# Kernel optimization log

Measured on AMD Instinct MI355X. Metric: run time of the kernel, lower is better.

Reference implementation:

```python
import jax, jax.numpy as jnp
import numpy as np

HEADS = 16
DIM_HEAD = 64
MAX_REL_POS = 1024   # temporal_length
TEXT_LEN = 77
IMG_SCALE = 1.0      # image_cross_attention_scale


def setup_inputs() -> dict:
    key = jax.random.key(0)
    ks = jax.random.split(key, 12)
    B, N, D = 32, 1024, 1024
    CTX = TEXT_LEN + 256
    s = 0.02
    return {
        "x": jax.random.normal(ks[0], (B, N, D), jnp.float32),
        "context": jax.random.normal(ks[1], (B, CTX, D), jnp.float32),
        "W_q": jax.random.normal(ks[2], (D, D), jnp.float32) * s,
        "W_k": jax.random.normal(ks[3], (D, D), jnp.float32) * s,
        "W_v": jax.random.normal(ks[4], (D, D), jnp.float32) * s,
        "W_k_ip": jax.random.normal(ks[5], (D, D), jnp.float32) * s,
        "W_v_ip": jax.random.normal(ks[6], (D, D), jnp.float32) * s,
        "rel_k": jax.random.normal(ks[7], (2 * MAX_REL_POS + 1, DIM_HEAD), jnp.float32) * s,
        "rel_v": jax.random.normal(ks[8], (2 * MAX_REL_POS + 1, DIM_HEAD), jnp.float32) * s,
        "W_out": jax.random.normal(ks[9], (D, D), jnp.float32) * s,
        "b_out": jnp.zeros((D,), jnp.float32),
        "alpha": jnp.zeros((1,), jnp.float32),
    }


def _split_heads(t):
    # [b, n, h*d] -> [b, h, n, d]
    b, n, _ = t.shape
    return t.reshape(b, n, HEADS, DIM_HEAD).transpose(0, 2, 1, 3)


def _merge_heads(t):
    # [b, h, n, d] -> [b, n, h*d]
    b, h, n, d = t.shape
    return t.transpose(0, 2, 1, 3).reshape(b, n, h * d)


def _rel_embeddings(table, len_q, len_k):
    # gather relative-position embeddings: [len_q, len_k, d]
    dist = jnp.arange(len_k)[None, :] - jnp.arange(len_q)[:, None]
    idx = jnp.clip(dist, -MAX_REL_POS, MAX_REL_POS) + MAX_REL_POS
    return table[idx]


def reference(x, context, W_q, W_k, W_v, W_k_ip, W_v_ip, rel_k, rel_v, W_out, b_out, alpha):
    scale = DIM_HEAD ** -0.5
    ctx_text = context[:, :TEXT_LEN, :]
    ctx_img = context[:, TEXT_LEN:, :]

    q = _split_heads(x @ W_q)          # [b,h,i,d]
    k = _split_heads(ctx_text @ W_k)   # [b,h,j,d]
    v = _split_heads(ctx_text @ W_v)

    sim = jnp.einsum('bhid,bhjd->bhij', q, k) * scale
    len_q, len_k = q.shape[2], k.shape[2]
    k2 = _rel_embeddings(rel_k, len_q, len_k)            # [i,j,d]
    sim = sim + jnp.einsum('bhid,ijd->bhij', q, k2) * scale
    attn = jax.nn.softmax(sim, axis=-1)

    out = jnp.einsum('bhij,bhjd->bhid', attn, v)
    v2 = _rel_embeddings(rel_v, len_q, len_k)            # [i,j,d]
    out = out + jnp.einsum('bhij,ijd->bhid', attn, v2)
    out = _merge_heads(out)                              # [b,i,h*d]

    # second image-context KV stream
    k_ip = _split_heads(ctx_img @ W_k_ip)
    v_ip = _split_heads(ctx_img @ W_v_ip)
    sim_ip = jnp.einsum('bhid,bhjd->bhij', q, k_ip) * scale
    attn_ip = jax.nn.softmax(sim_ip, axis=-1)
    out_ip = _merge_heads(jnp.einsum('bhij,bhjd->bhid', attn_ip, v_ip))

    # learnable-scale bypass: out + scale * out_ip * (tanh(alpha)+1)
    out = out + IMG_SCALE * out_ip * (jnp.tanh(alpha[0]) + 1.0)
    return out @ W_out + b_out
```

## Files before the change

### kernel.cpp

```cpp
#include <hip/hip_runtime.h>
#include <math.h>

typedef __bf16 bf16_t;
typedef __bf16 bf16x2 __attribute__((ext_vector_type(2)));
typedef __bf16 bf16x8 __attribute__((ext_vector_type(8)));
typedef float f32x4 __attribute__((ext_vector_type(4)));

#define BATCH   32
#define SEQ     1024
#define DMODEL  1024
#define NHEADS  16
#define DIMH    64
#define TEXTLEN 77
#define IMGLEN  256
#define CTXLEN  333
#define MAXREL  1024

#define MFMA16(a,b,c) __builtin_amdgcn_mfma_f32_16x16x32_bf16(a, b, c, 0, 0, 0)
#define SCALE_LOG2E 0.1803368809f

__device__ __forceinline__ unsigned pk2(float a, float b) {
  union { bf16x2 v; unsigned u; } t;
  t.v[0] = (bf16_t)a; t.v[1] = (bf16_t)b;
  return t.u;
}

__global__ __launch_bounds__(128) void k_cvt_ctx(const float* __restrict__ ctx,
                                                 bf16_t* __restrict__ ctxT,
                                                 bf16_t* __restrict__ ctxI) {
  int row = blockIdx.x;
  int b = row / CTXLEN, t = row - b * CTXLEN;
  const float* src = ctx + (size_t)row * DMODEL + threadIdx.x * 8;
  bf16_t* dst = (t < TEXTLEN)
      ? ctxT + ((size_t)(b * 80 + t)) * DMODEL + threadIdx.x * 8
      : ctxI + ((size_t)(b * IMGLEN + (t - TEXTLEN))) * DMODEL + threadIdx.x * 8;
  float4 a = *(const float4*)(src);
  float4 c = *(const float4*)(src + 4);
  bf16x8 o;
  o[0] = (bf16_t)a.x; o[1] = (bf16_t)a.y; o[2] = (bf16_t)a.z; o[3] = (bf16_t)a.w;
  o[4] = (bf16_t)c.x; o[5] = (bf16_t)c.y; o[6] = (bf16_t)c.z; o[7] = (bf16_t)c.w;
  *(bf16x8*)dst = o;
  if (t == 0) {
    bf16x8 z = {};
    #pragma unroll
    for (int rr = 77; rr < 80; ++rr)
      *(bf16x8*)(ctxT + ((size_t)(b * 80 + rr)) * DMODEL + threadIdx.x * 8) = z;
  }
}

__global__ void k_transpose_w(const float* __restrict__ W, bf16_t* __restrict__ WT) {
  __shared__ float tile[32][33];
  int x = threadIdx.x, y = threadIdx.y;
  int n0 = blockIdx.x * 32, k0 = blockIdx.y * 32;
  #pragma unroll
  for (int r = 0; r < 32; r += 8)
    tile[y + r][x] = W[(size_t)(k0 + y + r) * DMODEL + n0 + x];
  __syncthreads();
  #pragma unroll
  for (int r = 0; r < 32; r += 8)
    WT[(size_t)(n0 + y + r) * DMODEL + k0 + x] = (bf16_t)tile[x][y + r];
}

__global__ __launch_bounds__(256) void k_cvt_relk(const float* __restrict__ relk,
                                                  bf16_t* __restrict__ Rkb) {
  int idx = blockIdx.x * 256 + threadIdx.x;
  int u = idx >> 3, d0 = (idx & 7) * 8;
  const float* s = relk + (size_t)(u + 1) * DIMH + d0;
  float4 a = *(const float4*)s;
  float4 b = *(const float4*)(s + 4);
  bf16x8 o;
  o[0] = (bf16_t)a.x; o[1] = (bf16_t)a.y; o[2] = (bf16_t)a.z; o[3] = (bf16_t)a.w;
  o[4] = (bf16_t)b.x; o[5] = (bf16_t)b.y; o[6] = (bf16_t)b.z; o[7] = (bf16_t)b.w;
  *(bf16x8*)(Rkb + (size_t)u * DIMH + d0) = o;
}

__global__ __launch_bounds__(256) void k_cvt_relvT(const float* __restrict__ relv,
                                                   bf16_t* __restrict__ RvT) {
  int idx = blockIdx.x * 256 + threadIdx.x;
  int d = idx >> 8, u0 = (idx & 255) * 8;
  bf16x8 o;
  #pragma unroll
  for (int e = 0; e < 8; ++e)
    o[e] = (bf16_t)relv[(size_t)(u0 + e + 1) * DIMH + d];
  *(bf16x8*)(RvT + (size_t)d * 2048 + u0) = o;
}

typedef __attribute__((address_space(1))) void gvoid;
typedef __attribute__((address_space(3))) void svoid;

__device__ __forceinline__ void async_ld16(const void* g, void* l) {
  __builtin_amdgcn_global_load_lds((gvoid*)g, (svoid*)l, 16, 0, 0);
}

template<int STORE, bool AF32, bool AHM>
__global__ __launch_bounds__(256) void k_gemm(
    const void* __restrict__ Ain, const bf16_t* __restrict__ BT,
    void* __restrict__ Cout, void* __restrict__ Cout2,
    const float* __restrict__ bias, int M, int N, int K)
{
  constexpr int ABYTES = AF32 ? 16384 : 8192;
  __shared__ __align__(16) char lds_a[2][ABYTES];
  __shared__ __align__(16) bf16_t lds_b[2][128 * 32];
  const int tid = threadIdx.x;
  const int wid = tid >> 6, lane = tid & 63;
  const int nx = gridDim.x, ny = gridDim.y;
  const int lin = blockIdx.y * nx + blockIdx.x;
  const int nwg = nx * ny;
  const int swz = (lin & 7) * (nwg >> 3) + (lin >> 3);
  const int bcol = (swz % ny) * 128;
  const int brow = (swz / ny) * 128;
  const int wr = (wid >> 1) * 64, wc = (wid & 1) * 64;
  const int lhi = lane >> 4, llo = lane & 15;

  auto stage = [&](int kk, int buf) __attribute__((always_inline)) {
    char* la = lds_a[buf];
    if constexpr (AF32) {
      const float* A32 = (const float*)Ain;
      #pragma unroll
      for (int q = 0; q < 4; ++q) {
        int base = q * 4096 + wid * 1024;
        int L = base + lane * 16;
        int row = L >> 7, col16 = (L >> 4) & 7;
        async_ld16(A32 + (size_t)(brow + row) * K + kk + ((col16 ^ (row & 7)) << 2),
                   la + base);
      }
    } else if constexpr (AHM) {
      const bf16_t* A16 = (const bf16_t*)Ain;
      const int hh = kk >> 6;
      #pragma unroll
      for (int ch = 0; ch < 2; ++ch) {
        int e = wid * 512 + ch * 2048 + lane * 8;
        int row = e >> 5, col = e & 31;
        int grow = brow + row;
        const bf16_t* src = A16
            + (((size_t)((grow >> 10) * 16 + hh) * 1024 + (grow & 1023)) << 6)
            + (kk & 32) + col;
        async_ld16(src, la + (size_t)(wid * 512 + ch * 2048) * 2);
      }
    } else {
      const bf16_t* A16 = (const bf16_t*)Ain;
      #pragma unroll
      for (int ch = 0; ch < 2; ++ch) {
        int e = wid * 512 + ch * 2048 + lane * 8;
        int row = e >> 5, col = e & 31;
        async_ld16(A16 + (size_t)(brow + row) * K + kk + col,
                   la + (size_t)(wid * 512 + ch * 2048) * 2);
      }
    }
    bf16_t* lb = lds_b[buf];
    #pragma unroll
    for (int ch = 0; ch < 2; ++ch) {
      int e = wid * 512 + ch * 2048 + lane * 8;
      int row = e >> 5, col = e & 31;
      async_ld16(BT + (size_t)(bcol + row) * K + kk + col, &lb[wid * 512 + ch * 2048]);
    }
  };

  f32x4 acc[4][4];
  #pragma unroll
  for (int m = 0; m < 4; ++m)
    #pragma unroll
    for (int n = 0; n < 4; ++n)
      acc[m][n] = (f32x4){0.f, 0.f, 0.f, 0.f};

  stage(0, 0);
  int cur = 0;
  for (int kk = 0; kk < K; kk += 32) {
    if (kk + 32 < K) {
      stage(kk + 32, cur ^ 1);
      __builtin_amdgcn_sched_barrier(0);
      if constexpr (AF32)
        asm volatile("s_waitcnt vmcnt(6)" ::: "memory");
      else
        asm volatile("s_waitcnt vmcnt(4)" ::: "memory");
      __builtin_amdgcn_sched_barrier(0);
    } else {
      asm volatile("s_waitcnt vmcnt(0)" ::: "memory");
    }
    __builtin_amdgcn_s_barrier();

    bf16x8 af[4], bfv[4];
    if constexpr (AF32) {
      #pragma unroll
      for (int m = 0; m < 4; ++m) {
        int row = wr + m * 16 + llo;
        int sw = (llo & 7) << 4;
        const char* rp = lds_a[cur] + row * 128;
        f32x4 a0 = *(const f32x4*)(rp + (((lhi * 2) << 4) ^ sw));
        f32x4 a1 = *(const f32x4*)(rp + (((lhi * 2 + 1) << 4) ^ sw));
        bf16x8 v;
        v[0] = (bf16_t)a0[0]; v[1] = (bf16_t)a0[1]; v[2] = (bf16_t)a0[2]; v[3] = (bf16_t)a0[3];
        v[4] = (bf16_t)a1[0]; v[5] = (bf16_t)a1[1]; v[6] = (bf16_t)a1[2]; v[7] = (bf16_t)a1[3];
        af[m] = v;
      }
    } else {
      #pragma unroll
      for (int m = 0; m < 4; ++m)
        af[m] = *(const bf16x8*)(lds_a[cur] + (size_t)((wr + m * 16 + llo) * 32 + lhi * 8) * 2);
    }
    #pragma unroll
    for (int n = 0; n < 4; ++n)
      bfv[n] = *(const bf16x8*)&lds_b[cur][(wc + n * 16 + llo) * 32 + lhi * 8];
    #pragma unroll
    for (int m = 0; m < 4; ++m)
      #pragma unroll
      for (int n = 0; n < 4; ++n)
        acc[m][n] = MFMA16(af[m], bfv[n], acc[m][n]);

    asm volatile("s_waitcnt lgkmcnt(0)" ::: "memory");
    __builtin_amdgcn_sched_barrier(0);
    __builtin_amdgcn_s_barrier();
    cur ^= 1;
  }

  #pragma unroll
  for (int m = 0; m < 4; ++m)
    #pragma unroll
    for (int n = 0; n < 4; ++n) {
      const int gc = bcol + wc + n * 16 + llo;
      #pragma unroll
      for (int r = 0; r < 4; ++r) {
        const int gr = brow + wr + m * 16 + lhi * 4 + r;
        float v = acc[m][n][r];
        if constexpr (STORE == 2) {
          ((float*)Cout)[(size_t)gr * N + gc] = v + bias[gc];
        } else if constexpr (STORE == 4) {
          int hh2 = gc >> 6;
          ((bf16_t*)Cout)[((((size_t)((gr >> 10) * 16 + hh2)) << 10) + (gr & 1023)) * 64
                          + (gc & 63)] = (bf16_t)v;
        } else if constexpr (STORE == 5) {
          int bb = (gr * 6554) >> 19;
          int jj = gr - bb * 80;
          int hh2 = (gc & 1023) >> 6;
          bf16_t* dst = (gc < 1024) ? (bf16_t*)Cout : (bf16_t*)Cout2;
          dst[(((size_t)(bb * 16 + hh2) * 80 + jj) << 6) + (gc & 63)] = (bf16_t)v;
        } else {
          int bb = gr >> 8, uu = gr & 255;
          int hh2 = (gc & 1023) >> 6;
          bf16_t* dst = (gc < 1024) ? (bf16_t*)Cout : (bf16_t*)Cout2;
          dst[((((size_t)(bb * 16 + hh2)) << 8) + uu) * 64 + (gc & 63)] = (bf16_t)v;
        }
      }
    }
}

template<int RPB, int OUTC>
__global__ __launch_bounds__(256) void k_vtrans(const bf16_t* __restrict__ V,
                                                bf16_t* __restrict__ Vt) {
  __shared__ bf16_t tile[64][72];
  const int nt = (OUTC + 63) / 64;
  const int u0 = (blockIdx.x % nt) * 64;
  const int bh = blockIdx.x / nt;
  const int tid = threadIdx.x;
  const int ur = tid >> 2, cg = (tid & 3) * 16;
  {
    const bf16_t* src = V + (((size_t)bh * RPB + u0 + ur) << 6) + cg;
    *(bf16x8*)&tile[ur][cg] = *(const bf16x8*)src;
    *(bf16x8*)&tile[ur][cg + 8] = *(const bf16x8*)(src + 8);
  }
  __syncthreads();
  bf16x8 o0, o1;
  #pragma unroll
  for (int e = 0; e < 8; ++e) { o0[e] = tile[cg + e][ur]; o1[e] = tile[cg + 8 + e][ur]; }
  bf16_t* dst = Vt + (size_t)bh * 64 * OUTC + (size_t)ur * OUTC + u0 + cg;
  if (u0 + cg + 8 <= OUTC)  *(bf16x8*)dst = o0;
  if (u0 + cg + 16 <= OUTC) *(bf16x8*)(dst + 8) = o1;
}

__global__ __launch_bounds__(256, 2) void k_txt(
    const bf16_t* __restrict__ Qh,
    const bf16_t* __restrict__ Kth,
    const bf16_t* __restrict__ Vtt,
    const bf16_t* __restrict__ Rkb,
    const bf16_t* __restrict__ RvT,
    bf16_t* __restrict__ Oh)
{
  __shared__ __align__(16) bf16_t kt_l[80 * 64];
  __shared__ __align__(16) bf16_t vt_l[64 * 80];
  __shared__ __align__(16) char p_l[4][6400];
  __shared__ __align__(16) char qlds[4][2048];
  __shared__ __align__(16) char olds[4][2048];
  const int tid = threadIdx.x;
  const int w = tid >> 6, lane = tid & 63;
  const int c = lane & 15, g = lane >> 4;
  const int bh = blockIdx.x;

  #pragma unroll
  for (int q = 0; q < 3; ++q) {
    int cid0 = q * 256 + w * 64;
    if (cid0 < 640) {
      int cid = cid0 + lane;
      int row = cid >> 3, cc = cid & 7;
      const bf16_t* src = Kth + (((size_t)bh * 80 + row) << 6) + ((cc ^ (row & 7)) << 3);
      async_ld16(src, (char*)kt_l + cid0 * 16);
    }
  }
  #pragma unroll
  for (int q = 0; q < 3; ++q) {
    int cid0 = q * 256 + w * 64;
    if (cid0 < 640) {
      int cid = cid0 + lane;
      int row = cid / 10;
      int col = cid - row * 10;
      int colp = col - (row & 7); if (colp < 0) colp += 10;
      const bf16_t* src = Vtt + (size_t)bh * 5120 + row * 80 + colp * 8;
      async_ld16(src, (char*)vt_l + cid0 * 16);
    }
  }
  {
    int iq = w * 256;
    #pragma unroll
    for (int k2 = 0; k2 < 2; ++k2) {
      int k = k2 * 64 + lane, rr = k >> 3, cc = k & 7;
      async_ld16(Qh + (((size_t)bh * 1024 + iq + rr) << 6) + ((cc ^ (rr & 7)) << 3),
                 qlds[w] + k2 * 1024);
    }
  }
  __syncthreads();

  bf16_t* p = (bf16_t*)p_l[w];

  for (int st = 0; st < 16; ++st) {
    const int iq = w * 256 + st * 16;
    const int ub = 1008 - iq;
    asm volatile("s_waitcnt vmcnt(0)" ::: "memory");
    bf16x8 qa0 = *(const bf16x8*)(qlds[w] + c * 128 + ((g ^ (c & 7)) << 4));
    bf16x8 qa1 = *(const bf16x8*)(qlds[w] + c * 128 + (((g + 4) ^ (c & 7)) << 4));
    asm volatile("s_waitcnt lgkmcnt(0)" ::: "memory");
    if (st < 15) {
      int iqn = iq + 16;
      #pragma unroll
      for (int k2 = 0; k2 < 2; ++k2) {
        int k = k2 * 64 + lane, rr = k >> 3, cc = k & 7;
        async_ld16(Qh + (((size_t)bh * 1024 + iqn + rr) << 6) + ((cc ^ (rr & 7)) << 3),
                   qlds[w] + k2 * 1024);
      }
    }
    f32x4 ta[6];
    #pragma unroll
    for (int n = 0; n < 6; ++n) ta[n] = (f32x4){0.f, 0.f, 0.f, 0.f};
    {
      const bf16_t* rp = Rkb + (size_t)(ub + c) * DIMH + g * 8;
      #pragma unroll
      for (int n = 0; n < 6; ++n) {
        bf16x8 b0 = *(const bf16x8*)(rp + n * 16 * DIMH);
        bf16x8 b1 = *(const bf16x8*)(rp + n * 16 * DIMH + 32);
        ta[n] = MFMA16(qa0, b0, ta[n]);
        ta[n] = MFMA16(qa1, b1, ta[n]);
      }
    }
    f32x4 s[5];
    #pragma unroll
    for (int n = 0; n < 5; ++n) s[n] = (f32x4){0.f, 0.f, 0.f, 0.f};
    {
      const int sw = (c & 7) << 4;
      #pragma unroll
      for (int n = 0; n < 5; ++n) {
        int rb = (n * 16 + c) * 128;
        bf16x8 k0 = *(const bf16x8*)((const char*)kt_l + rb + ((g << 4) ^ sw));
        bf16x8 k1 = *(const bf16x8*)((const char*)kt_l + rb + (((4 + g) << 4) ^ sw));
        s[n] = MFMA16(qa0, k0, s[n]);
        s[n] = MFMA16(qa1, k1, s[n]);
      }
    }
    float st4[5][4];
    #pragma unroll
    for (int r = 0; r < 4; ++r) {
      int il = 4 * g + r;
      int cz = c + 15 - il;
      int srcl = (lane & 48) | (cz & 15);
      bool lo_pick = (cz >> 4) == 0;
      #pragma unroll
      for (int n = 0; n < 5; ++n) {
        float tlo = __shfl(ta[n][r], srcl);
        float thi = __shfl(ta[n + 1][r], srcl);
        float tv = lo_pick ? tlo : thi;
        int j = 16 * n + c;
        st4[n][r] = (j < TEXTLEN) ? (s[n][r] + tv) : -1e30f;
      }
    }
    float rsum[4];
    #pragma unroll
    for (int r = 0; r < 4; ++r) {
      float m = st4[0][r];
      #pragma unroll
      for (int n = 1; n < 5; ++n) m = fmaxf(m, st4[n][r]);
      m = fmaxf(m, __shfl_xor(m, 1));
      m = fmaxf(m, __shfl_xor(m, 2));
      m = fmaxf(m, __shfl_xor(m, 4));
      m = fmaxf(m, __shfl_xor(m, 8));
      float ssum = 0.f;
      #pragma unroll
      for (int n = 0; n < 5; ++n) {
        float pv = exp2f((st4[n][r] - m) * SCALE_LOG2E);
        st4[n][r] = pv;
        ssum += pv;
      }
      ssum += __shfl_xor(ssum, 1);
      ssum += __shfl_xor(ssum, 2);
      ssum += __shfl_xor(ssum, 4);
      ssum += __shfl_xor(ssum, 8);
      rsum[r] = ssum;
    }
    {
      bf16x8 z8 = {};
      #pragma unroll
      for (int z = 0; z < 7; ++z) {
        int off = z * 1024 + lane * 16;
        if (off < 6400)
          *(bf16x8*)((char*)p + off) = z8;
      }
      #pragma unroll
      for (int n = 0; n < 5; ++n)
        #pragma unroll
        for (int r = 0; r < 4; ++r) {
          int j = 16 * n + c;
          if (j < TEXTLEN) {
            int il = 4 * g + r;
            bf16_t pb = (bf16_t)st4[n][r];
            p[il * 200 + (j + 15 - il)] = pb;
            p[il * 200 + 96 + j] = pb;
          }
        }
    }
    f32x4 ot[4];
    #pragma unroll
    for (int dt = 0; dt < 4; ++dt) ot[dt] = (f32x4){0.f, 0.f, 0.f, 0.f};
    #pragma unroll
    for (int kt = 0; kt < 6; ++kt) {
      bf16x8 pf = *(const bf16x8*)(p + c * 200 + kt * 32 + g * 8);
      int klo = kt * 32 + g * 8;
      #pragma unroll
      for (int dt = 0; dt < 4; ++dt) {
        int d = dt * 16 + c;
        bf16x8 af;
        if (klo < 96) {
          af = *(const bf16x8*)(RvT + (size_t)d * 2048 + ub + klo);
        } else {
          int uv = klo - 96;
          int chunk = (uv >> 3) + (c & 7); if (chunk >= 10) chunk -= 10;
          af = *(const bf16x8*)((const char*)vt_l + d * 160 + chunk * 16);
        }
        ot[dt] = MFMA16(af, pf, ot[dt]);
      }
    }
    int srcq = ((c >> 2) << 4) | c;
    float t0 = __shfl(rsum[0], srcq);
    float t1 = __shfl(rsum[1], srcq);
    float t2 = __shfl(rsum[2], srcq);
    float t3 = __shfl(rsum[3], srcq);
    float rs = (c & 2) ? ((c & 1) ? t3 : t2) : ((c & 1) ? t1 : t0);
    float inv = 1.f / rs;
    #pragma unroll
    for (int dt = 0; dt < 4; ++dt) {
      int chunk = dt * 2 + (g >> 1);
      char* pa = olds[w] + c * 128 + ((chunk ^ (c & 7)) << 4) + (g & 1) * 8;
      uint2 nv;
      nv.x = pk2(ot[dt][0] * inv, ot[dt][1] * inv);
      nv.y = pk2(ot[dt][2] * inv, ot[dt][3] * inv);
      *(uint2*)pa = nv;
    }
    char* ob = (char*)(Oh + (((size_t)bh * 1024 + iq) << 6));
    #pragma unroll
    for (int k2 = 0; k2 < 2; ++k2) {
      int k = k2 * 64 + lane, rr = k >> 3, cc = k & 7;
      uint4 v = *(uint4*)(olds[w] + rr * 128 + ((cc ^ (rr & 7)) << 4));
      *(uint4*)(ob + rr * 128 + cc * 16) = v;
    }
  }
}

__global__ __launch_bounds__(256, 2) void k_img(
    const bf16_t* __restrict__ Qh,
    const bf16_t* __restrict__ Khi,
    const bf16_t* __restrict__ Vipt,
    const float* __restrict__ alpha,
    bf16_t* __restrict__ Oh)
{
  __shared__ __align__(16) bf16_t kst[256 * 64];
  __shared__ __align__(16) bf16_t vst[64 * 256];
  __shared__ __align__(16) char qlds[4][2048];
  __shared__ __align__(16) char olds[4][2048];
  const int tid = threadIdx.x;
  const int w = tid >> 6, lane = tid & 63;
  const int c = lane & 15, g = lane >> 4;
  const int i0 = blockIdx.x * 512;
  const int bh = blockIdx.y;

  #pragma unroll
  for (int q = 0; q < 8; ++q) {
    int cid = q * 256 + tid;
    int row = cid >> 3, cc = cid & 7;
    const bf16_t* src = Khi + (((size_t)bh * 256 + row) << 6) + ((cc ^ (row & 7)) << 3);
    async_ld16(src, (char*)kst + q * 4096 + w * 1024);
  }
  const char* vsrc0 = (const char*)(Vipt + (size_t)bh * 16384);
  #pragma unroll
  for (int q = 0; q < 8; ++q) {
    int L = (q * 256 + tid) * 16;
    int row = L >> 9;
    async_ld16(vsrc0 + (L ^ ((row & 7) << 4)), (char*)vst + q * 4096 + w * 1024);
  }
  {
    int iq = i0 + w * 128;
    #pragma unroll
    for (int k2 = 0; k2 < 2; ++k2) {
      int k = k2 * 64 + lane, rr = k >> 3, cc = k & 7;
      size_t off = (((size_t)bh * 1024 + iq + rr) << 6) + ((cc ^ (rr & 7)) << 3);
      async_ld16(Qh + off, qlds[w] + k2 * 1024);
      async_ld16(Oh + off, olds[w] + k2 * 1024);
    }
  }
  __syncthreads();

  const float coef = tanhf(alpha[0]) + 1.0f;

  for (int st = 0; st < 8; ++st) {
    const int iq = i0 + w * 128 + st * 16;
    asm volatile("s_waitcnt vmcnt(0)" ::: "memory");
    bf16x8 qa0 = *(const bf16x8*)(qlds[w] + c * 128 + ((g ^ (c & 7)) << 4));
    bf16x8 qa1 = *(const bf16x8*)(qlds[w] + c * 128 + (((g + 4) ^ (c & 7)) << 4));
    asm volatile("s_waitcnt lgkmcnt(0)" ::: "memory");
    if (st < 7) {
      int iqn = iq + 16;
      #pragma unroll
      for (int k2 = 0; k2 < 2; ++k2) {
        int k = k2 * 64 + lane, rr = k >> 3, cc = k & 7;
        async_ld16(Qh + (((size_t)bh * 1024 + iqn + rr) << 6) + ((cc ^ (rr & 7)) << 3),
                   qlds[w] + k2 * 1024);
      }
    }
    f32x4 acc[4];
    #pragma unroll
    for (int dt = 0; dt < 4; ++dt) acc[dt] = (f32x4){0.f, 0.f, 0.f, 0.f};
    float m_run = -1e30f, l_run = 0.f;

    #pragma unroll
    for (int jt = 0; jt < 2; ++jt) {
      f32x4 s2[8];
      #pragma unroll
      for (int n = 0; n < 8; ++n) s2[n] = (f32x4){0.f, 0.f, 0.f, 0.f};
      const int sw = (c & 7) << 4;
      #pragma unroll
      for (int n = 0; n < 8; ++n) {
        int rb = (jt * 128 + n * 16 + c) * 128;
        bf16x8 k0 = *(const bf16x8*)((const char*)kst + rb + ((g << 4) ^ sw));
        bf16x8 k1 = *(const bf16x8*)((const char*)kst + rb + (((4 + g) << 4) ^ sw));
        s2[n] = MFMA16(k0, qa0, s2[n]);
        s2[n] = MFMA16(k1, qa1, s2[n]);
      }
      float mx = -1e30f;
      #pragma unroll
      for (int n = 0; n < 8; ++n)
        #pragma unroll
        for (int r = 0; r < 4; ++r) mx = fmaxf(mx, s2[n][r]);
      mx = fmaxf(mx, __shfl_xor(mx, 16));
      mx = fmaxf(mx, __shfl_xor(mx, 32));
      float m_new = fmaxf(m_run, mx);
      float fscale = exp2f((m_run - m_new) * SCALE_LOG2E);
      float tsum = 0.f;
      #pragma unroll
      for (int n = 0; n < 8; ++n)
        #pragma unroll
        for (int r = 0; r < 4; ++r) {
          float pv = exp2f((s2[n][r] - m_new) * SCALE_LOG2E);
          s2[n][r] = pv; tsum += pv;
        }
      tsum += __shfl_xor(tsum, 16);
      tsum += __shfl_xor(tsum, 32);
      l_run = l_run * fscale + tsum;
      m_run = m_new;
      #pragma unroll
      for (int dt = 0; dt < 4; ++dt) acc[dt] *= fscale;
      const int srcA = c | ((g & 1) << 5);
      const int srcB = srcA + 16;
      const bool hi_n = ((g >> 1) & 1) != 0;
      #pragma unroll
      for (int kt = 0; kt < 4; ++kt) {
        unsigned lo0 = pk2(s2[2 * kt][0], s2[2 * kt][1]);
        unsigned hi0 = pk2(s2[2 * kt][2], s2[2 * kt][3]);
        unsigned lo1 = pk2(s2[2 * kt + 1][0], s2[2 * kt + 1][1]);
        unsigned hi1 = pk2(s2[2 * kt + 1][2], s2[2 * kt + 1][3]);
        unsigned a0 = __shfl(lo0, srcA), a1 = __shfl(lo1, srcA);
        unsigned b0 = __shfl(hi0, srcA), b1 = __shfl(hi1, srcA);
        unsigned c0 = __shfl(lo0, srcB), c1 = __shfl(lo1, srcB);
        unsigned d0 = __shfl(hi0, srcB), d1 = __shfl(hi1, srcB);
        union { unsigned u[4]; bf16x8 v; } pf;
        pf.u[0] = hi_n ? a1 : a0;
        pf.u[1] = hi_n ? b1 : b0;
        pf.u[2] = hi_n ? c1 : c0;
        pf.u[3] = hi_n ? d1 : d0;
        #pragma unroll
        for (int dt = 0; dt < 4; ++dt) {
          int d = dt * 16 + c;
          int a = (d * 512 + jt * 256 + kt * 64 + g * 16) ^ ((c & 7) << 4);
          bf16x8 vf = *(const bf16x8*)((const char*)vst + a);
          acc[dt] = MFMA16(vf, pf.v, acc[dt]);
        }
      }
    }
    float inv = coef / l_run;
    asm volatile("s_waitcnt vmcnt(0)" ::: "memory");
    #pragma unroll
    for (int dt = 0; dt < 4; ++dt) {
      int chunk = dt * 2 + (g >> 1);
      char* pa = olds[w] + c * 128 + ((chunk ^ (c & 7)) << 4) + (g & 1) * 8;
      union { uint2 u2; bf16_t e[4]; } ov; ov.u2 = *(uint2*)pa;
      uint2 nv;
      nv.x = pk2((float)ov.e[0] + acc[dt][0] * inv, (float)ov.e[1] + acc[dt][1] * inv);
      nv.y = pk2((float)ov.e[2] + acc[dt][2] * inv, (float)ov.e[3] + acc[dt][3] * inv);
      *(uint2*)pa = nv;
    }
    char* ob = (char*)(Oh + (((size_t)bh * 1024 + iq) << 6));
    #pragma unroll
    for (int k2 = 0; k2 < 2; ++k2) {
      int k = k2 * 64 + lane, rr = k >> 3, cc = k & 7;
      uint4 v = *(uint4*)(olds[w] + rr * 128 + ((cc ^ (rr & 7)) << 4));
      *(uint4*)(ob + rr * 128 + cc * 16) = v;
    }
    asm volatile("s_waitcnt lgkmcnt(0)" ::: "memory");
    if (st < 7) {
      int iqn = iq + 16;
      #pragma unroll
      for (int k2 = 0; k2 < 2; ++k2) {
        int k = k2 * 64 + lane, rr = k >> 3, cc = k & 7;
        async_ld16(Oh + (((size_t)bh * 1024 + iqn + rr) << 6) + ((cc ^ (rr & 7)) << 3),
                   olds[w] + k2 * 1024);
      }
    }
  }
}

extern "C" void kernel_launch(void* const* d_in, const int* in_sizes, int n_in,
                              void* d_out, int out_size, void* d_ws, size_t ws_size,
                              hipStream_t stream)
{
  const float* x     = (const float*)d_in[0];
  const float* ctx   = (const float*)d_in[1];
  const float* W_q   = (const float*)d_in[2];
  const float* W_k   = (const float*)d_in[3];
  const float* W_v   = (const float*)d_in[4];
  const float* W_kip = (const float*)d_in[5];
  const float* W_vip = (const float*)d_in[6];
  const float* rel_k = (const float*)d_in[7];
  const float* rel_v = (const float*)d_in[8];
  const float* W_out = (const float*)d_in[9];
  const float* b_out = (const float*)d_in[10];
  const float* alpha = (const float*)d_in[11];

  char* ws = (char*)d_ws;
  bf16_t* Oh   = (bf16_t*)(ws + 0);
  bf16_t* Qh   = (bf16_t*)(ws + 67108864);
  bf16_t* CtxT = (bf16_t*)(ws + 134217728);
  bf16_t* CtxI = (bf16_t*)(ws + 139460608);
  bf16_t* WTs  = (bf16_t*)(ws + 156237824);
  bf16_t* WqT   = WTs + 0 * 1048576;
  bf16_t* WkT   = WTs + 1 * 1048576;
  bf16_t* WvT   = WTs + 2 * 1048576;
  bf16_t* WkipT = WTs + 3 * 1048576;
  bf16_t* WvipT = WTs + 4 * 1048576;
  bf16_t* WoutT = WTs + 5 * 1048576;

  char* dob = (char*)d_out;
  bf16_t* Khi   = (bf16_t*)(dob + 0);
  bf16_t* Vhi   = (bf16_t*)(dob + 16777216);
  bf16_t* Vipt  = (bf16_t*)(dob + 33554432);
  bf16_t* Kth   = (bf16_t*)(dob + 50331648);
  bf16_t* Vth   = (bf16_t*)(dob + 55574528);
  bf16_t* Vtt   = (bf16_t*)(dob + 60817408);
  bf16_t* Rkb   = (bf16_t*)(dob + 66060288);
  bf16_t* RvT   = (bf16_t*)(dob + 66322432);

  k_cvt_ctx<<<BATCH * CTXLEN, 128, 0, stream>>>(ctx, CtxT, CtxI);
  dim3 tb(32, 8), tg(32, 32);
  k_transpose_w<<<tg, tb, 0, stream>>>(W_q,   WqT);
  k_transpose_w<<<tg, tb, 0, stream>>>(W_k,   WkT);
  k_transpose_w<<<tg, tb, 0, stream>>>(W_v,   WvT);
  k_transpose_w<<<tg, tb, 0, stream>>>(W_kip, WkipT);
  k_transpose_w<<<tg, tb, 0, stream>>>(W_vip, WvipT);
  k_transpose_w<<<tg, tb, 0, stream>>>(W_out, WoutT);
  k_cvt_relk<<<64, 256, 0, stream>>>(rel_k, Rkb);
  k_cvt_relvT<<<64, 256, 0, stream>>>(rel_v, RvT);

  k_gemm<4, true,  false><<<dim3(256, 8), 256, 0, stream>>>(x, WqT, (void*)Qh, nullptr, nullptr, 32768, 1024, 1024);
  k_gemm<5, false, false><<<dim3(20, 16), 256, 0, stream>>>(CtxT, WkT,   (void*)Kth, (void*)Vth, nullptr, 2560, 2048, 1024);
  k_gemm<6, false, false><<<dim3(64, 16), 256, 0, stream>>>(CtxI, WkipT, (void*)Khi, (void*)Vhi, nullptr, 8192, 2048, 1024);

  k_vtrans<80,  80 ><<<2 * 512, 256, 0, stream>>>(Vth, Vtt);
  k_vtrans<256, 256><<<4 * 512, 256, 0, stream>>>(Vhi, Vipt);

  k_txt<<<512, 256, 0, stream>>>(Qh, Kth, Vtt, Rkb, RvT, Oh);
  k_img<<<dim3(2, 512), 256, 0, stream>>>(Qh, Khi, Vipt, alpha, Oh);

  k_gemm<2, false, true><<<dim3(256, 8), 256, 0, stream>>>(Oh, WoutT, d_out, nullptr, b_out, 32768, 1024, 1024);
}
```

Measured before the change: 569.5 us.

## Enlarge GEMM tiles to 256x128 with 8 waves, swizzled LDS, pre-converted bf16 x

The GEMM kernel now uses 512-thread workgroups computing 256x128 output tiles, so each B tile is reused across twice as many rows. The LDS layout for A and B gets an XOR swizzle on 16-byte chunks, meant to cut bank conflicts on the fragment reads. The fp32 A path that converted inside the GEMM is removed. x is instead converted to bf16 by a separate kernel into scratch space in the output buffer, which adds an extra read and write pass over x. The grids are halved to match the new tile size, which lowers the workgroup count and may hurt occupancy or tail balance on the smaller K/V GEMMs.

```diff
diff --git a/kernel.cpp b/kernel.cpp
--- a/kernel.cpp
+++ b/kernel.cpp
@@ -23,6 +23,17 @@
   union { bf16x2 v; unsigned u; } t;
   t.v[0] = (bf16_t)a; t.v[1] = (bf16_t)b;
   return t.u;
+}
+
+__global__ __launch_bounds__(256) void k_cvt_x(const float* __restrict__ in,
+                                               bf16_t* __restrict__ out) {
+  size_t idx = ((size_t)blockIdx.x * blockDim.x + threadIdx.x) * 8;
+  float4 a = *(const float4*)(in + idx);
+  float4 b = *(const float4*)(in + idx + 4);
+  bf16x8 o;
+  o[0] = (bf16_t)a.x; o[1] = (bf16_t)a.y; o[2] = (bf16_t)a.z; o[3] = (bf16_t)a.w;
+  o[4] = (bf16_t)b.x; o[5] = (bf16_t)b.y; o[6] = (bf16_t)b.z; o[7] = (bf16_t)b.w;
+  *(bf16x8*)(out + idx) = o;
 }
 
 __global__ __launch_bounds__(128) void k_cvt_ctx(const float* __restrict__ ctx,
@@ -92,14 +103,13 @@
   __builtin_amdgcn_global_load_lds((gvoid*)g, (svoid*)l, 16, 0, 0);
 }
 
-template<int STORE, bool AF32, bool AHM>
-__global__ __launch_bounds__(256) void k_gemm(
-    const void* __restrict__ Ain, const bf16_t* __restrict__ BT,
+template<int STORE, bool AHM>
+__global__ __launch_bounds__(512) void k_gemm(
+    const bf16_t* __restrict__ A16, const bf16_t* __restrict__ BT,
     void* __restrict__ Cout, void* __restrict__ Cout2,
     const float* __restrict__ bias, int M, int N, int K)
 {
-  constexpr int ABYTES = AF32 ? 16384 : 8192;
-  __shared__ __align__(16) char lds_a[2][ABYTES];
+  __shared__ __align__(16) bf16_t lds_a[2][256 * 32];
   __shared__ __align__(16) bf16_t lds_b[2][128 * 32];
   const int tid = threadIdx.x;
   const int wid = tid >> 6, lane = tid & 63;
@@ -108,51 +118,31 @@
   const int nwg = nx * ny;
   const int swz = (lin & 7) * (nwg >> 3) + (lin >> 3);
   const int bcol = (swz % ny) * 128;
-  const int brow = (swz / ny) * 128;
+  const int brow = (swz / ny) * 256;
   const int wr = (wid >> 1) * 64, wc = (wid & 1) * 64;
   const int lhi = lane >> 4, llo = lane & 15;
 
   auto stage = [&](int kk, int buf) __attribute__((always_inline)) {
-    char* la = lds_a[buf];
-    if constexpr (AF32) {
-      const float* A32 = (const float*)Ain;
-      #pragma unroll
-      for (int q = 0; q < 4; ++q) {
-        int base = q * 4096 + wid * 1024;
-        int L = base + lane * 16;
-        int row = L >> 7, col16 = (L >> 4) & 7;
-        async_ld16(A32 + (size_t)(brow + row) * K + kk + ((col16 ^ (row & 7)) << 2),
-                   la + base);
-      }
-    } else if constexpr (AHM) {
-      const bf16_t* A16 = (const bf16_t*)Ain;
-      const int hh = kk >> 6;
-      #pragma unroll
-      for (int ch = 0; ch < 2; ++ch) {
-        int e = wid * 512 + ch * 2048 + lane * 8;
-        int row = e >> 5, col = e & 31;
+    #pragma unroll
+    for (int ch = 0; ch < 2; ++ch) {
+      int cid = ch * 512 + tid;
+      int row = cid >> 2, ccol = cid & 3;
+      int gcol = (ccol ^ (row & 3)) << 3;
+      const bf16_t* src;
+      if constexpr (AHM) {
         int grow = brow + row;
-        const bf16_t* src = A16
-            + (((size_t)((grow >> 10) * 16 + hh) * 1024 + (grow & 1023)) << 6)
-            + (kk & 32) + col;
-        async_ld16(src, la + (size_t)(wid * 512 + ch * 2048) * 2);
-      }
-    } else {
-      const bf16_t* A16 = (const bf16_t*)Ain;
-      #pragma unroll
-      for (int ch = 0; ch < 2; ++ch) {
-        int e = wid * 512 + ch * 2048 + lane * 8;
-        int row = e >> 5, col = e & 31;
-        async_ld16(A16 + (size_t)(brow + row) * K + kk + col,
-                   la + (size_t)(wid * 512 + ch * 2048) * 2);
-      }
-    }
-    bf16_t* lb = lds_b[buf];
-    #pragma unroll
-    for (int ch = 0; ch < 2; ++ch) {
-      int e = wid * 512 + ch * 2048 + lane * 8;
-      int row = e >> 5, col = e & 31;
-      async_ld16(BT + (size_t)(bcol + row) * K + kk + col, &lb[wid * 512 + ch * 2048]);
+        src = A16 + (((size_t)((grow >> 10) * 16 + (kk >> 6)) * 1024 + (grow & 1023)) << 6)
+              + (kk & 32) + gcol;
+      } else {
+        src = A16 + (size_t)(brow + row) * K + kk + gcol;
+      }
+      async_ld16(src, (char*)lds_a[buf] + cid * 16);
+    }
+    {
+      int row = tid >> 2, ccol = tid & 3;
+      int gcol = (ccol ^ (row & 3)) << 3;
+      async_ld16(BT + (size_t)(bcol + row) * K + kk + gcol,
+                 (char*)lds_b[buf] + tid * 16);
     }
   };
 
@@ -169,10 +159,7 @@
     if (kk + 32 < K) {
       stage(kk + 32, cur ^ 1);
       __builtin_amdgcn_sched_barrier(0);
-      if constexpr (AF32)
-        asm volatile("s_waitcnt vmcnt(6)" ::: "memory");
-      else
-        asm volatile("s_waitcnt vmcnt(4)" ::: "memory");
+      asm volatile("s_waitcnt vmcnt(3)" ::: "memory");
       __builtin_amdgcn_sched_barrier(0);
     } else {
       asm volatile("s_waitcnt vmcnt(0)" ::: "memory");
@@ -180,27 +167,18 @@
     __builtin_amdgcn_s_barrier();
 
     bf16x8 af[4], bfv[4];
-    if constexpr (AF32) {
-      #pragma unroll
-      for (int m = 0; m < 4; ++m) {
-        int row = wr + m * 16 + llo;
-        int sw = (llo & 7) << 4;
-        const char* rp = lds_a[cur] + row * 128;
-        f32x4 a0 = *(const f32x4*)(rp + (((lhi * 2) << 4) ^ sw));
-        f32x4 a1 = *(const f32x4*)(rp + (((lhi * 2 + 1) << 4) ^ sw));
-        bf16x8 v;
-        v[0] = (bf16_t)a0[0]; v[1] = (bf16_t)a0[1]; v[2] = (bf16_t)a0[2]; v[3] = (bf16_t)a0[3];
-        v[4] = (bf16_t)a1[0]; v[5] = (bf16_t)a1[1]; v[6] = (bf16_t)a1[2]; v[7] = (bf16_t)a1[3];
-        af[m] = v;
-      }
-    } else {
-      #pragma unroll
-      for (int m = 0; m < 4; ++m)
-        af[m] = *(const bf16x8*)(lds_a[cur] + (size_t)((wr + m * 16 + llo) * 32 + lhi * 8) * 2);
-    }
-    #pragma unroll
-    for (int n = 0; n < 4; ++n)
-      bfv[n] = *(const bf16x8*)&lds_b[cur][(wc + n * 16 + llo) * 32 + lhi * 8];
+    #pragma unroll
+    for (int m = 0; m < 4; ++m) {
+      int row = wr + m * 16 + llo;
+      af[m] = *(const bf16x8*)((const char*)lds_a[cur] + row * 64
+                               + ((lhi ^ (row & 3)) << 4));
+    }
+    #pragma unroll
+    for (int n = 0; n < 4; ++n) {
+      int row = wc + n * 16 + llo;
+      bfv[n] = *(const bf16x8*)((const char*)lds_b[cur] + row * 64
+                                + ((lhi ^ (row & 3)) << 4));
+    }
     #pragma unroll
     for (int m = 0; m < 4; ++m)
       #pragma unroll
@@ -670,7 +648,9 @@
   bf16_t* Vtt   = (bf16_t*)(dob + 60817408);
   bf16_t* Rkb   = (bf16_t*)(dob + 66060288);
   bf16_t* RvT   = (bf16_t*)(dob + 66322432);
-
+  bf16_t* Xb    = (bf16_t*)(dob + 66584576);
+
+  k_cvt_x<<<16384, 256, 0, stream>>>(x, Xb);
   k_cvt_ctx<<<BATCH * CTXLEN, 128, 0, stream>>>(ctx, CtxT, CtxI);
   dim3 tb(32, 8), tg(32, 32);
   k_transpose_w<<<tg, tb, 0, stream>>>(W_q,   WqT);
@@ -682,9 +662,9 @@
   k_cvt_relk<<<64, 256, 0, stream>>>(rel_k, Rkb);
   k_cvt_relvT<<<64, 256, 0, stream>>>(rel_v, RvT);
 
-  k_gemm<4, true,  false><<<dim3(256, 8), 256, 0, stream>>>(x, WqT, (void*)Qh, nullptr, nullptr, 32768, 1024, 1024);
-  k_gemm<5, false, false><<<dim3(20, 16), 256, 0, stream>>>(CtxT, WkT,   (void*)Kth, (void*)Vth, nullptr, 2560, 2048, 1024);
-  k_gemm<6, false, false><<<dim3(64, 16), 256, 0, stream>>>(CtxI, WkipT, (void*)Khi, (void*)Vhi, nullptr, 8192, 2048, 1024);
+  k_gemm<4, false><<<dim3(128, 8),  512, 0, stream>>>(Xb,   WqT,   (void*)Qh,  nullptr,     nullptr, 32768, 1024, 1024);
+  k_gemm<5, false><<<dim3(10, 16),  512, 0, stream>>>(CtxT, WkT,   (void*)Kth, (void*)Vth,  nullptr, 2560,  2048, 1024);
+  k_gemm<6, false><<<dim3(32, 16),  512, 0, stream>>>(CtxI, WkipT, (void*)Khi, (void*)Vhi,  nullptr, 8192,  2048, 1024);
 
   k_vtrans<80,  80 ><<<2 * 512, 256, 0, stream>>>(Vth, Vtt);
   k_vtrans<256, 256><<<4 * 512, 256, 0, stream>>>(Vhi, Vipt);
@@ -692,5 +672,5 @@
   k_txt<<<512, 256, 0, stream>>>(Qh, Kth, Vtt, Rkb, RvT, Oh);
   k_img<<<dim3(2, 512), 256, 0, stream>>>(Qh, Khi, Vipt, alpha, Oh);
 
-  k_gemm<2, false, true><<<dim3(256, 8), 256, 0, stream>>>(Oh, WoutT, d_out, nullptr, b_out, 32768, 1024, 1024);
-}
+  k_gemm<2, true><<<dim3(128, 8), 512, 0, stream>>>(Oh, WoutT, d_out, nullptr, b_out, 32768, 1024, 1024);
+}
```

Measured after the change: 529.5 us. 7.0% less time.
